# Performance work log

Measured on AMD Instinct MI355X. Metric: run time of the kernel, lower is better.

The kernel has to match this reference:

```python
import jax, jax.numpy as jnp
import numpy as np
from functools import partial

VOCAB = 50000
D_EMB = 256
D_HID = 512            # bidirectional output size
H = D_HID // 2         # per-direction hidden = 256
NT = 24                # number of tags (incl START/STOP)
START = 22
STOP = 23
L = 4096               # sentence length
NEG = -1.0e6


def setup_inputs() -> dict:
    key = jax.random.key(0)
    ks = jax.random.split(key, 16)
    g = lambda k, shp, sc=0.1: (jax.random.normal(k, shp, dtype=jnp.float32) * sc)
    sentence = jax.random.randint(ks[0], (L,), 0, VOCAB)
    h0 = jax.random.normal(ks[1], (2, 1, H), dtype=jnp.float32)
    c0 = jax.random.normal(ks[2], (2, 1, H), dtype=jnp.float32)
    emb = g(ks[3], (VOCAB, D_EMB), 1.0)
    # torch nn.LSTM weights: gate order [i, f, g, o], 4H rows
    W_ih_f = g(ks[4], (4 * H, D_EMB)); W_hh_f = g(ks[5], (4 * H, H))
    b_ih_f = g(ks[6], (4 * H,));       b_hh_f = g(ks[7], (4 * H,))
    W_ih_b = g(ks[8], (4 * H, D_EMB)); W_hh_b = g(ks[9], (4 * H, H))
    b_ih_b = g(ks[10], (4 * H,));      b_hh_b = g(ks[11], (4 * H,))
    W_out = g(ks[12], (NT, D_HID));    b_out = g(ks[13], (NT,))
    transitions = jax.random.normal(ks[14], (NT, NT), dtype=jnp.float32)
    transitions = transitions.at[START, :].set(NEG).at[:, STOP].set(NEG)
    return dict(sentence=sentence, h0=h0, c0=c0, emb=emb,
                W_ih_f=W_ih_f, W_hh_f=W_hh_f, b_ih_f=b_ih_f, b_hh_f=b_hh_f,
                W_ih_b=W_ih_b, W_hh_b=W_hh_b, b_ih_b=b_ih_b, b_hh_b=b_hh_b,
                W_out=W_out, b_out=b_out, transitions=transitions)


def _lstm_scan(x_proj, h0, c0, W_hh):
    # x_proj: [L, 4H] = x @ W_ih.T + b_ih + b_hh (input part precomputed)
    def step(carry, xp):
        h, c = carry
        gates = xp + W_hh @ h                       # [4H]
        i, f, gg, o = jnp.split(gates, 4)
        i = jax.nn.sigmoid(i); f = jax.nn.sigmoid(f)
        gg = jnp.tanh(gg);     o = jax.nn.sigmoid(o)
        c = f * c + i * gg
        h = o * jnp.tanh(c)
        return (h, c), h
    _, hs = jax.lax.scan(step, (h0, c0), x_proj)
    return hs  # [L, H]


def reference(sentence, h0, c0, emb,
              W_ih_f, W_hh_f, b_ih_f, b_hh_f,
              W_ih_b, W_hh_b, b_ih_b, b_hh_b,
              W_out, b_out, transitions):
    x = emb[sentence]                                # [L, D_EMB]
    # forward direction
    xp_f = x @ W_ih_f.T + (b_ih_f + b_hh_f)          # [L, 4H]
    hs_f = _lstm_scan(xp_f, h0[0, 0], c0[0, 0], W_hh_f)
    # backward direction (scan reversed sequence, then flip back)
    xp_b = x[::-1] @ W_ih_b.T + (b_ih_b + b_hh_b)
    hs_b = _lstm_scan(xp_b, h0[1, 0], c0[1, 0], W_hh_b)[::-1]
    lstm_out = jnp.concatenate([hs_f, hs_b], axis=-1)  # [L, D_HID]
    feats = lstm_out @ W_out.T + b_out                 # [L, NT]

    # Viterbi decode, vectorized over tags; transitions[next, prev]
    init = jnp.full((NT,), NEG, dtype=feats.dtype).at[START].set(0.0)

    def vstep(fv, feat):
        scores = fv[None, :] + transitions             # [NT(next), NT(prev)]
        best_prev = jnp.argmax(scores, axis=1)         # [NT]
        fv_new = jnp.max(scores, axis=1) + feat
        return fv_new, best_prev

    fv, bptrs = jax.lax.scan(vstep, init, feats)       # bptrs: [L, NT]
    terminal = fv + transitions[STOP]
    best_last = jnp.argmax(terminal)
    path_score = terminal[best_last]

    def back(tag, bp):
        return bp[tag], tag
    _, best_path = jax.lax.scan(back, best_last, bptrs, reverse=True)  # [L]
    return path_score, best_path
```

## Files before the change

kernel.cpp:

```cpp
#include <hip/hip_runtime.h>
#include <math.h>

#define SLEN 4096
#define DEMB 256
#define HDIM 256
#define G4   1024
#define NT   24
#define TAG_START 22
#define TAG_STOP  23
#define NEGV (-1.0e6f)
#define NINF (-3.0e38f)

#define OFF_XP    0
#define OFF_LSTM  33554432
#define OFF_FEATS 41943040
#define OFF_BP    42336256
#define OFF_MAPS  42733568
#define OFF_EVEC  42739712
#define OFF_BLAST 42739968

__device__ __forceinline__ float sigm_f(float x) {
    return 1.0f / (1.0f + __expf(-x));
}
__device__ __forceinline__ float tanh_f(float x) {
    return 1.0f - 2.0f / (__expf(2.0f * x) + 1.0f);
}

__global__ __launch_bounds__(512) void init_zero_kernel(unsigned long long* __restrict__ p)
{
    int i = blockIdx.x * 512 + threadIdx.x;
    if (i < 2048) p[i] = 0ull;
}

__global__ __launch_bounds__(256) void xp_gemm_kernel(
    const int* __restrict__ sent, const float* __restrict__ emb,
    const float* __restrict__ W_ih_f, const float* __restrict__ b_ih_f, const float* __restrict__ b_hh_f,
    const float* __restrict__ W_ih_b, const float* __restrict__ b_ih_b, const float* __restrict__ b_hh_b,
    float* __restrict__ xp)
{
    const int bx = blockIdx.x;
    const int tt = bx & 63;
    const int rt = bx >> 6;
    const int rowbase = rt * 64;
    const int dir = rowbase >> 10;
    const int rib = rowbase & 1023;
    const float* W  = dir ? W_ih_b : W_ih_f;
    const float* bi = dir ? b_ih_b : b_ih_f;
    const float* bh = dir ? b_hh_b : b_hh_f;
    const int tid = threadIdx.x;

    __shared__ int sl[64];
    __shared__ __align__(16) float xs[16][64];
    __shared__ __align__(16) float wsd[16][64];
    if (tid < 64) sl[tid] = sent[tt * 64 + tid];
    __syncthreads();

    float acc[4][4];
#pragma unroll
    for (int i = 0; i < 4; i++)
#pragma unroll
        for (int j = 0; j < 4; j++) acc[i][j] = 0.f;

    const int tl = tid >> 2, kq = tid & 3;
    const int tr = tid >> 4, rc = tid & 15;
    const int t0 = tr * 4, r0 = rc * 4;

    for (int kb = 0; kb < 256; kb += 16) {
        float4 xv = *(const float4*)(emb + (size_t)sl[tl] * DEMB + kb + kq * 4);
        float4 wv = *(const float4*)(W + (size_t)(rib + tl) * DEMB + kb + kq * 4);
        xs[kq*4+0][tl] = xv.x; xs[kq*4+1][tl] = xv.y; xs[kq*4+2][tl] = xv.z; xs[kq*4+3][tl] = xv.w;
        wsd[kq*4+0][tl] = wv.x; wsd[kq*4+1][tl] = wv.y; wsd[kq*4+2][tl] = wv.z; wsd[kq*4+3][tl] = wv.w;
        __syncthreads();
#pragma unroll
        for (int k = 0; k < 16; k++) {
            float4 a = *(const float4*)&xs[k][t0];
            float4 b = *(const float4*)&wsd[k][r0];
            acc[0][0] += a.x*b.x; acc[0][1] += a.x*b.y; acc[0][2] += a.x*b.z; acc[0][3] += a.x*b.w;
            acc[1][0] += a.y*b.x; acc[1][1] += a.y*b.y; acc[1][2] += a.y*b.z; acc[1][3] += a.y*b.w;
            acc[2][0] += a.z*b.x; acc[2][1] += a.z*b.y; acc[2][2] += a.z*b.z; acc[2][3] += a.z*b.w;
            acc[3][0] += a.w*b.x; acc[3][1] += a.w*b.y; acc[3][2] += a.w*b.z; acc[3][3] += a.w*b.w;
        }
        __syncthreads();
    }

#pragma unroll
    for (int jj = 0; jj < 4; jj++) {
        float bsum = bi[rib + r0 + jj] + bh[rib + r0 + jj];
        acc[0][jj] += bsum; acc[1][jj] += bsum; acc[2][jj] += bsum; acc[3][jj] += bsum;
    }
#pragma unroll
    for (int i = 0; i < 4; i++) {
        int t = tt * 64 + t0 + i;
        float4 o; o.x = acc[i][0]; o.y = acc[i][1]; o.z = acc[i][2]; o.w = acc[i][3];
        *(float4*)(xp + ((size_t)dir * SLEN + t) * G4 + rib + r0) = o;
    }
}

__global__ __launch_bounds__(512) void lstm_scan_kernel(
    const float* __restrict__ xp, const float* __restrict__ h0, const float* __restrict__ c0,
    const float* __restrict__ W_hh_f, const float* __restrict__ W_hh_b,
    float* __restrict__ lstm_out,
    unsigned long long* __restrict__ hfast, unsigned long long* __restrict__ hpub)
{
    const int bx = blockIdx.x;
    const int sub = bx & 7;
    if (sub >= 2) return;
    const int dir = sub;
    const int s = bx >> 3;
    const int tid = threadIdx.x;

    const int wave = tid >> 6, lane = tid & 63;
    const int q = wave & 3, rgrp = wave >> 2;
    const int row_local = rgrp * 64 + lane;
    const int row_global = ((row_local >> 5) << 8) + s * 32 + (row_local & 31);

    __shared__ __align__(16) float h_lds[256];
    __shared__ float red[128][5];

    const float* Whh = dir ? W_hh_b : W_hh_f;
    float wreg[64];
    {
        const float4* wr = (const float4*)(Whh + (size_t)row_global * HDIM + q * 64);
#pragma unroll
        for (int i = 0; i < 16; i++) {
            float4 v = wr[i];
            wreg[4*i] = v.x; wreg[4*i+1] = v.y; wreg[4*i+2] = v.z; wreg[4*i+3] = v.w;
        }
    }

    const int own_lo = s * 32;
    const int gt = tid - own_lo;
    const bool is_gate = (gt >= 0) && (gt < 32);

    float c_state = 0.f;
    float xp4[4] = {0.f, 0.f, 0.f, 0.f};
    if (is_gate) {
        c_state = c0[dir * HDIM + own_lo + gt];
        int tpos0 = dir ? (SLEN - 1) : 0;
        const float* base = xp + ((size_t)dir * SLEN + tpos0) * G4;
#pragma unroll
        for (int g = 0; g < 4; g++) xp4[g] = base[(g << 8) + own_lo + gt];
    }

    int use_fast = 1, miss_cnt = 0;

    for (int t = 0; t < SLEN; ++t) {
        if (tid < 256) {
            if (t == 0) {
                h_lds[tid] = h0[dir * HDIM + tid];
            } else if (!is_gate) {
                const unsigned want = (unsigned)t;
                const int par = t & 1;
                unsigned long long v = 0;
                int got = 0;
                if (use_fast) {
                    const unsigned long long* pf = hfast + dir * 256 + par * 512 + tid;
#pragma unroll 1
                    for (int k = 0; k < 16; ++k) {
                        unsigned long long fv;
                        asm volatile("global_load_dwordx2 %0, %1, off sc0\n\t"
                                     "s_waitcnt vmcnt(0)"
                                     : "=&v"(fv) : "v"(pf) : "memory");
                        if ((unsigned)(fv >> 32) == want) { v = fv; got = 1; break; }
                    }
                    if (!got && ++miss_cnt > 128) use_fast = 0;
                }
                if (!got) {
                    const unsigned long long* pa = hpub + dir * 256 + par * 512 + tid;
                    do {
                        v = __hip_atomic_load(pa, __ATOMIC_RELAXED, __HIP_MEMORY_SCOPE_AGENT);
                    } while ((unsigned)(v >> 32) != want);
                }
                h_lds[tid] = __uint_as_float((unsigned)(v & 0xffffffffull));
            }
        }
        __syncthreads();

        float a0 = 0.f, a1 = 0.f, a2 = 0.f, a3 = 0.f;
        {
            const float4* h4 = (const float4*)&h_lds[q * 64];
#pragma unroll
            for (int i = 0; i < 16; i++) {
                float4 hv = h4[i];
                a0 += wreg[4*i]   * hv.x;
                a1 += wreg[4*i+1] * hv.y;
                a2 += wreg[4*i+2] * hv.z;
                a3 += wreg[4*i+3] * hv.w;
            }
        }
        red[row_local][q] = (a0 + a1) + (a2 + a3);
        __syncthreads();

        if (is_gate) {
            float pre[4];
#pragma unroll
            for (int g = 0; g < 4; g++) {
                int rl = g * 32 + gt;
                pre[g] = ((red[rl][0] + red[rl][1]) + (red[rl][2] + red[rl][3])) + xp4[g];
            }
            float iv  = sigm_f(pre[0]);
            float fvv = sigm_f(pre[1]);
            float gv  = tanh_f(pre[2]);
            float ov  = sigm_f(pre[3]);
            c_state = fvv * c_state + iv * gv;
            float h = ov * tanh_f(c_state);
            int hglob = own_lo + gt;
            int tpos = dir ? (SLEN - 1 - t) : t;
            lstm_out[(size_t)tpos * 512 + dir * HDIM + hglob] = h;
            h_lds[hglob] = h;
            const unsigned tag = (unsigned)(t + 1);
            const int ppar = (t + 1) & 1;
            unsigned long long pv = ((unsigned long long)tag << 32)
                                  | (unsigned long long)__float_as_uint(h);
            unsigned long long* pf = hfast + dir * 256 + ppar * 512 + hglob;
            asm volatile("global_store_dwordx2 %0, %1, off"
                         :: "v"(pf), "v"(pv) : "memory");
            __hip_atomic_store(hpub + dir * 256 + ppar * 512 + hglob, pv,
                               __ATOMIC_RELAXED, __HIP_MEMORY_SCOPE_AGENT);
            if ((t + 1) < SLEN) {
                int tpos1 = dir ? (SLEN - 2 - t) : (t + 1);
                const float* base = xp + ((size_t)dir * SLEN + tpos1) * G4;
#pragma unroll
                for (int g = 0; g < 4; g++) xp4[g] = base[(g << 8) + own_lo + gt];
            }
        }
    }
}

__global__ __launch_bounds__(256) void feats_kernel(
    const float* __restrict__ lstm, const float* __restrict__ W_out,
    const float* __restrict__ b_out, float* __restrict__ feats)
{
    int gid = blockIdx.x * 256 + threadIdx.x;
    if (gid >= SLEN * NT) return;
    int t = gid / NT, n = gid - t * NT;
    const float4* hr = (const float4*)(lstm + (size_t)t * 512);
    const float4* wr = (const float4*)(W_out + (size_t)n * 512);
    float acc = 0.f;
#pragma unroll 8
    for (int k = 0; k < 128; k++) {
        float4 a = hr[k], b = wr[k];
        acc += a.x * b.x + a.y * b.y + a.z * b.z + a.w * b.w;
    }
    feats[gid] = acc + b_out[n];
}

__global__ __launch_bounds__(64) void viterbi_fwd_kernel(
    const float* __restrict__ feats, const float* __restrict__ trans,
    int* __restrict__ bp, float* __restrict__ score_out, int* __restrict__ blast)
{
    int lane = threadIdx.x;
    __shared__ __align__(16) float fvs[32];
    float Trow[NT];
    float tstop = NINF;
    float fv;
    if (lane < NT) {
#pragma unroll
        for (int p = 0; p < NT; p++) Trow[p] = trans[lane * NT + p];
        tstop = trans[TAG_STOP * NT + lane];
        fv = (lane == TAG_START) ? 0.f : NEGV;
    } else {
        fv = NINF;
#pragma unroll
        for (int p = 0; p < NT; p++) Trow[p] = NINF;
    }
    float fnext = (lane < NT) ? feats[lane] : 0.f;
    for (int t = 0; t < SLEN; t++) {
        float featv = fnext;
        if ((t + 1) < SLEN && lane < NT) fnext = feats[(t + 1) * NT + lane];
        if (lane < NT) fvs[lane] = fv;
        __syncthreads();
        float best = NINF; int arg = 0;
#pragma unroll
        for (int pq = 0; pq < 6; pq++) {
            float4 f4 = *(const float4*)&fvs[pq * 4];
            float sc;
            sc = f4.x + Trow[pq*4+0]; if (sc > best) { best = sc; arg = pq*4+0; }
            sc = f4.y + Trow[pq*4+1]; if (sc > best) { best = sc; arg = pq*4+1; }
            sc = f4.z + Trow[pq*4+2]; if (sc > best) { best = sc; arg = pq*4+2; }
            sc = f4.w + Trow[pq*4+3]; if (sc > best) { best = sc; arg = pq*4+3; }
        }
        if (lane < NT) bp[t * NT + lane] = arg;
        fv = best + featv;
    }
    float term = (lane < NT) ? (fv + tstop) : NINF;
    int idx = lane;
#pragma unroll
    for (int off = 32; off >= 1; off >>= 1) {
        float v2 = __shfl_xor(term, off);
        int   i2 = __shfl_xor(idx, off);
        if (v2 > term || (v2 == term && i2 < idx)) { term = v2; idx = i2; }
    }
    if (lane == 0) { score_out[0] = term; blast[0] = idx; }
}

__global__ __launch_bounds__(64) void bt_maps_kernel(
    const int* __restrict__ bp, int* __restrict__ maps)
{
    int c = blockIdx.x;
    __shared__ int bpl[64 * NT];
    for (int idx = threadIdx.x; idx < 64 * NT; idx += 64) bpl[idx] = bp[c * 64 * NT + idx];
    __syncthreads();
    if (threadIdx.x < NT) {
        int f = threadIdx.x;
#pragma unroll 1
        for (int k = 63; k >= 0; k--) f = bpl[k * NT + f];
        maps[c * NT + threadIdx.x] = f;
    }
}

__global__ __launch_bounds__(64) void bt_combine_kernel(
    const int* __restrict__ maps, const int* __restrict__ blast, int* __restrict__ evec)
{
    __shared__ int ml[64 * NT];
    for (int idx = threadIdx.x; idx < 64 * NT; idx += 64) ml[idx] = maps[idx];
    __syncthreads();
    if (threadIdx.x == 0) {
        int e = blast[0];
        evec[63] = e;
        for (int c = 63; c >= 1; c--) { e = ml[c * NT + e]; evec[c - 1] = e; }
    }
}

__global__ __launch_bounds__(64) void bt_emit_kernel(
    const int* __restrict__ bp, const int* __restrict__ evec, float* __restrict__ out_path)
{
    int c = blockIdx.x;
    __shared__ int bpl[64 * NT];
    for (int idx = threadIdx.x; idx < 64 * NT; idx += 64) bpl[idx] = bp[c * 64 * NT + idx];
    __syncthreads();
    if (threadIdx.x == 0) {
        int f = evec[c];
        out_path[c * 64 + 63] = (float)f;
        for (int t = 62; t >= 0; t--) {
            f = bpl[(t + 1) * NT + f];
            out_path[c * 64 + t] = (float)f;
        }
    }
}

extern "C" void kernel_launch(void* const* d_in, const int* in_sizes, int n_in,
                              void* d_out, int out_size, void* d_ws, size_t ws_size,
                              hipStream_t stream)
{
    const int*   sent   = (const int*)d_in[0];
    const float* h0     = (const float*)d_in[1];
    const float* c0     = (const float*)d_in[2];
    const float* emb    = (const float*)d_in[3];
    const float* W_ih_f = (const float*)d_in[4];
    const float* W_hh_f = (const float*)d_in[5];
    const float* b_ih_f = (const float*)d_in[6];
    const float* b_hh_f = (const float*)d_in[7];
    const float* W_ih_b = (const float*)d_in[8];
    const float* W_hh_b = (const float*)d_in[9];
    const float* b_ih_b = (const float*)d_in[10];
    const float* b_hh_b = (const float*)d_in[11];
    const float* W_out  = (const float*)d_in[12];
    const float* b_out  = (const float*)d_in[13];
    const float* trans  = (const float*)d_in[14];

    char* ws = (char*)d_ws;
    float* xp    = (float*)(ws + OFF_XP);
    float* lstm  = (float*)(ws + OFF_LSTM);
    float* feats = (float*)(ws + OFF_FEATS);
    int*   bp    = (int*)  (ws + OFF_BP);
    unsigned long long* hfast = (unsigned long long*)(ws + OFF_BP);
    unsigned long long* hpub  = (unsigned long long*)(ws + OFF_BP + 8192);
    int*   maps  = (int*)  (ws + OFF_MAPS);
    int*   evec  = (int*)  (ws + OFF_EVEC);
    int*   blast = (int*)  (ws + OFF_BLAST);

    float* outf = (float*)d_out;

    init_zero_kernel<<<4, 512, 0, stream>>>(hfast);
    xp_gemm_kernel<<<2048, 256, 0, stream>>>(sent, emb, W_ih_f, b_ih_f, b_hh_f,
                                             W_ih_b, b_ih_b, b_hh_b, xp);
    lstm_scan_kernel<<<64, 512, 0, stream>>>(xp, h0, c0, W_hh_f, W_hh_b, lstm, hfast, hpub);
    feats_kernel<<<384, 256, 0, stream>>>(lstm, W_out, b_out, feats);
    viterbi_fwd_kernel<<<1, 64, 0, stream>>>(feats, trans, bp, outf, blast);
    bt_maps_kernel<<<64, 64, 0, stream>>>(bp, maps);
    bt_combine_kernel<<<1, 64, 0, stream>>>(maps, blast, evec);
    bt_emit_kernel<<<64, 64, 0, stream>>>(bp, evec, outf + 1);
}
```

Before: 7.538 ms.

## Place all LSTM scan blocks on one XCC via runtime XCC-ID election

```diff
diff --git a/kernel.cpp b/kernel.cpp
--- a/kernel.cpp
+++ b/kernel.cpp
@@ -29,7 +29,7 @@
 __global__ __launch_bounds__(512) void init_zero_kernel(unsigned long long* __restrict__ p)
 {
     int i = blockIdx.x * 512 + threadIdx.x;
-    if (i < 2048) p[i] = 0ull;
+    if (i < 2056) p[i] = 0ull;
 }
 
 __global__ __launch_bounds__(256) void xp_gemm_kernel(
@@ -100,14 +100,39 @@
     const float* __restrict__ xp, const float* __restrict__ h0, const float* __restrict__ c0,
     const float* __restrict__ W_hh_f, const float* __restrict__ W_hh_b,
     float* __restrict__ lstm_out,
-    unsigned long long* __restrict__ hfast, unsigned long long* __restrict__ hpub)
-{
-    const int bx = blockIdx.x;
-    const int sub = bx & 7;
-    if (sub >= 2) return;
-    const int dir = sub;
-    const int s = bx >> 3;
+    unsigned long long* __restrict__ hfast, unsigned long long* __restrict__ hpub,
+    int* __restrict__ ctrl)
+{
     const int tid = threadIdx.x;
+
+    __shared__ int role_sh;
+    if (tid == 0) {
+        unsigned xcc;
+        asm volatile("s_getreg_b32 %0, hwreg(HW_REG_XCC_ID)" : "=s"(xcc));
+        xcc &= 7u;
+        int slot = __hip_atomic_fetch_add(&ctrl[xcc], 1,
+                                          __ATOMIC_RELAXED, __HIP_MEMORY_SCOPE_AGENT);
+        int role = -1;
+        if (slot < 16) {
+            if (slot == 15) {
+                int expect = 0;
+                __hip_atomic_compare_exchange_strong(&ctrl[8], &expect, (int)xcc + 1,
+                    __ATOMIC_RELAXED, __ATOMIC_RELAXED, __HIP_MEMORY_SCOPE_AGENT);
+            }
+            int w;
+            do {
+                w = __hip_atomic_load(&ctrl[8], __ATOMIC_RELAXED, __HIP_MEMORY_SCOPE_AGENT);
+            } while (w == 0);
+            if (w == (int)xcc + 1) role = slot;
+        }
+        role_sh = role;
+    }
+    __syncthreads();
+    const int role = role_sh;
+    if (role < 0) return;
+
+    const int dir = role >> 3;
+    const int s   = role & 7;
 
     const int wave = tid >> 6, lane = tid & 63;
     const int q = wave & 3, rgrp = wave >> 2;
@@ -366,16 +391,18 @@
     int*   bp    = (int*)  (ws + OFF_BP);
     unsigned long long* hfast = (unsigned long long*)(ws + OFF_BP);
     unsigned long long* hpub  = (unsigned long long*)(ws + OFF_BP + 8192);
+    int* ctrl = (int*)(ws + OFF_BP + 16384);
     int*   maps  = (int*)  (ws + OFF_MAPS);
     int*   evec  = (int*)  (ws + OFF_EVEC);
     int*   blast = (int*)  (ws + OFF_BLAST);
 
     float* outf = (float*)d_out;
 
-    init_zero_kernel<<<4, 512, 0, stream>>>(hfast);
+    init_zero_kernel<<<5, 512, 0, stream>>>(hfast);
     xp_gemm_kernel<<<2048, 256, 0, stream>>>(sent, emb, W_ih_f, b_ih_f, b_hh_f,
                                              W_ih_b, b_ih_b, b_hh_b, xp);
-    lstm_scan_kernel<<<64, 512, 0, stream>>>(xp, h0, c0, W_hh_f, W_hh_b, lstm, hfast, hpub);
+    lstm_scan_kernel<<<128, 512, 0, stream>>>(xp, h0, c0, W_hh_f, W_hh_b, lstm,
+                                              hfast, hpub, ctrl);
     feats_kernel<<<384, 256, 0, stream>>>(lstm, W_out, b_out, feats);
     viterbi_fwd_kernel<<<1, 64, 0, stream>>>(feats, trans, bp, outf, blast);
     bt_maps_kernel<<<64, 64, 0, stream>>>(bp, maps);
```

Measured after the change: 7.707 ms. +2.2%, slower.
